# Kernel optimization log

Hardware: AMD Instinct MI355X
Metric: run time of the kernel (lower is better)

The kernel has to match this reference:

```python
import jax, jax.numpy as jnp
import numpy as np

B = 8; N_PER = 4096; N = B * N_PER          # batched graph: 8 graphs x 4096 nodes
DEG = 8; E_PER = N_PER * DEG; E = B * E_PER  # 262144 edges total
H = 128; LAYERS = 15; IN_F = 3; OUT_F = 1; EPS = 1e-5


def setup_inputs() -> dict:
    key = jax.random.key(0)
    ks = jax.random.split(key, 8)
    x = jax.random.normal(ks[0], (N, IN_F), jnp.float32)
    off = (jnp.arange(B) * N_PER)[:, None]  # keep edges within each graph
    src = (jax.random.randint(ks[1], (B, E_PER), 0, N_PER) + off).reshape(-1).astype(jnp.int32)
    dst = (jax.random.randint(ks[2], (B, E_PER), 0, N_PER) + off).reshape(-1).astype(jnp.int32)
    L = jax.random.normal(ks[3], (E,), jnp.float32) * 0.1  # Laplacian edge weights
    mask = jnp.ones((N, 1), jnp.float32)
    nb = 2 * LAYERS  # 30 inner GraphConv1x1 layers, all [2H -> H]
    W1 = jax.random.normal(ks[4], (IN_F, H), jnp.float32) * (1.0 / np.sqrt(IN_F))
    b1 = jnp.zeros((H,), jnp.float32)
    Wb = jax.random.normal(ks[5], (nb, 2 * H, H), jnp.float32) * (1.0 / np.sqrt(2 * H))
    bb = jnp.zeros((nb, H), jnp.float32)
    gb = jnp.ones((nb, 2 * H), jnp.float32)
    betab = jnp.zeros((nb, 2 * H), jnp.float32)
    g2 = jnp.ones((H,), jnp.float32)
    beta2 = jnp.zeros((H,), jnp.float32)
    W2 = jax.random.normal(ks[6], (H, OUT_F), jnp.float32) * (1.0 / np.sqrt(H))
    b2 = jnp.zeros((OUT_F,), jnp.float32)
    return {"x": x, "L": L, "mask": mask, "W1": W1, "b1": b1, "Wb": Wb, "bb": bb,
            "gb": gb, "betab": betab, "g2": g2, "beta2": beta2, "W2": W2, "b2": b2,
            "src": src, "dst": dst}


def _bn(h, g, b):
    # BatchNorm1d in training mode: per-channel stats over all nodes (B*N_PER)
    m = h.mean(axis=0)
    v = jnp.mean((h - m) ** 2, axis=0)
    return (h - m) * (g / jnp.sqrt(v + EPS)) + b


def reference(x, L, mask, W1, b1, Wb, bb, gb, betab, g2, beta2, W2, b2, src, dst):
    def spmm(h):  # update_all(u_mul_e('feat','L'), sum('msg','feat'))
        return jax.ops.segment_sum(h[src] * L[:, None], dst, num_segments=N)

    def gavg(h):  # masked per-graph global average, broadcast back to nodes
        s = (h * mask).reshape(B, N_PER, -1).sum(axis=1)   # [B, C]
        n = mask.reshape(B, N_PER, 1).sum(axis=1)           # [B, 1]
        return jnp.repeat(s / n, N_PER, axis=0)             # [N, C]

    h = x @ W1 + b1  # conv1: no BN
    for i in range(LAYERS):
        res = h
        for j in range(2):
            k = 2 * i + j
            h = jax.nn.elu(h)
            agg = spmm(h) if i % 2 == 0 else gavg(h)
            h = jnp.concatenate([h, agg], axis=1)           # [N, 2H]
            h = _bn(h, gb[k], betab[k])                     # pre-BN
            h = h @ Wb[k] + bb[k]                           # [N, H]
        h = h + res
    h = jax.nn.elu(h)
    h = _bn(h, g2, beta2)
    h = h @ W2 + b2
    # repeating_expand(in=3, out=1) -> inputs[:, :1]
    return h + x[:, :OUT_F]
```

## Files before the change

kernel.cpp:

```cpp
#include <hip/hip_runtime.h>
#include <hip/hip_bf16.h>
#include <math.h>

#define NTOT   32768
#define NPER   4096
#define NGRAPH 8
#define EDGES  262144
#define HCH    128
#define EPSBN  1e-5f
#define BANKS  16

typedef short bf16x8 __attribute__((ext_vector_type(8)));
typedef float f32x4  __attribute__((ext_vector_type(4)));

__device__ __forceinline__ float eluf(float x){ return x > 0.f ? x : expm1f(x); }
__device__ __forceinline__ ushort f2bf(float f){
    uint u = __float_as_uint(f);
    u += 0x7fffu + ((u >> 16) & 1u);
    return (ushort)(u >> 16);
}
__device__ __forceinline__ float bfhi(uint p){ return __uint_as_float(p & 0xffff0000u); }
__device__ __forceinline__ float bflo(uint p){ return __uint_as_float(p << 16); }
__device__ __forceinline__ uint packu(float v){
    ushort hi = f2bf(v);
    float r = v - __uint_as_float(((uint)hi) << 16);
    ushort lo = f2bf(r);
    return (((uint)hi) << 16) | (uint)lo;
}

__global__ __launch_bounds__(256) void k_hist(const int* __restrict__ dst, int* __restrict__ deg){
    int e = blockIdx.x * 256 + threadIdx.x;
    atomicAdd(&deg[dst[e]], 1);
}

__global__ __launch_bounds__(1024) void k_scan(const int* __restrict__ deg, int* __restrict__ rowptr,
                                               int* __restrict__ cursor){
    __shared__ int part[1024];
    int t = threadIdx.x;
    const int chunk = NTOT / 1024;
    int base = t * chunk;
    int s = 0;
    for (int j = 0; j < chunk; ++j) s += deg[base + j];
    part[t] = s; __syncthreads();
    for (int off = 1; off < 1024; off <<= 1){
        int v = (t >= off) ? part[t - off] : 0;
        __syncthreads();
        part[t] += v;
        __syncthreads();
    }
    int run = part[t] - s;
    for (int j = 0; j < chunk; ++j){
        rowptr[base + j] = run; cursor[base + j] = run;
        run += deg[base + j];
    }
    if (t == 1023) rowptr[NTOT] = run;
}

__global__ __launch_bounds__(256) void k_scatter(const int* __restrict__ src, const int* __restrict__ dst,
                                                 const float* __restrict__ L, int* __restrict__ cursor,
                                                 int2* __restrict__ epk){
    int e = blockIdx.x * 256 + threadIdx.x;
    int d = dst[e];
    int pos = atomicAdd(&cursor[d], 1);
    int2 pv; pv.x = src[e]; pv.y = __float_as_int(L[e]);
    epk[pos] = pv;
}

__global__ __launch_bounds__(256) void k_cnt(const float* __restrict__ mask, float* __restrict__ gcnt){
    __shared__ float red[4];
    int g = blockIdx.x, t = threadIdx.x;
    float s = 0.f;
    for (int i = t; i < NPER; i += 256) s += mask[g * NPER + i];
    #pragma unroll
    for (int off = 32; off > 0; off >>= 1) s += __shfl_down(s, off);
    if ((t & 63) == 0) red[t >> 6] = s;
    __syncthreads();
    if (t == 0) gcnt[g] = red[0] + red[1] + red[2] + red[3];
}

__global__ __launch_bounds__(256) void k_wall(const float* __restrict__ Wb, uint4* __restrict__ Braw){
    int layer = blockIdx.x >> 4;
    int it = ((blockIdx.x & 15) << 8) | threadIdx.x;
    int nt = it >> 9;
    int rem = it & 511;
    int kc = rem >> 6, l = rem & 63;
    int col = nt * 16 + (l & 15);
    int k0  = kc * 32 + (l >> 4) * 8;
    const float* W = Wb + (size_t)layer * 256 * HCH;
    ushort hi[8];
    #pragma unroll
    for (int q = 0; q < 8; ++q) hi[q] = f2bf(W[(size_t)(k0 + q) * HCH + col]);
    uint4 vh;
    vh.x = hi[0] | ((uint)hi[1] << 16); vh.y = hi[2] | ((uint)hi[3] << 16);
    vh.z = hi[4] | ((uint)hi[5] << 16); vh.w = hi[6] | ((uint)hi[7] << 16);
    Braw[(size_t)layer * 4096 + (size_t)(nt * 8 + kc) * 64 + l] = vh;
}

__global__ __launch_bounds__(256) void k_conv1(const float* __restrict__ x, const float* __restrict__ W1,
                                               const float* __restrict__ b1, float* __restrict__ H,
                                               uint* __restrict__ Upk, ushort* __restrict__ Uh,
                                               float* __restrict__ sums0){
    __shared__ float red[2][2][128];
    int t = threadIdx.x, ch = t & 127, pr = t >> 7;
    float w0 = W1[ch], w1 = W1[128 + ch], w2 = W1[256 + ch], bv = b1[ch];
    int base = blockIdx.x * 128;
    float ls = 0.f, lss = 0.f;
    for (int it = 0; it < 64; ++it){
        int row = base + 2 * it + pr;
        const float* xr = x + (size_t)row * 3;
        float h = fmaf(xr[2], w2, fmaf(xr[1], w1, fmaf(xr[0], w0, bv)));
        H[(size_t)row * HCH + ch] = h;
        float u = eluf(h);
        uint p = packu(u);
        Upk[(size_t)row * HCH + ch] = p;
        Uh[(size_t)row * HCH + ch] = (ushort)(p >> 16);
        ls += u; lss += u * u;
    }
    red[0][pr][ch] = ls; red[1][pr][ch] = lss;
    __syncthreads();
    if (t < 128){
        float* sb_ = sums0 + (size_t)(blockIdx.x & (BANKS - 1)) * 512;
        atomicAdd(&sb_[t],       red[0][0][t] + red[0][1][t]);
        atomicAdd(&sb_[256 + t], red[1][0][t] + red[1][1][t]);
    }
}

__global__ __launch_bounds__(256) void k_spmm(const ushort* __restrict__ Uh, const int* __restrict__ rowptr,
                                              const int2* __restrict__ epk,
                                              ushort* __restrict__ AGGh, float* __restrict__ sums_k){
    __shared__ float red[2][16][128];
    const int t = threadIdx.x;
    const int rg = t >> 4, c8 = (t & 15) << 3;
    const int bid = blockIdx.x;
    const int sb = ((bid & 7) << 8) | (bid >> 3);
    const int node = sb * 16 + rg;
    const int e0 = rowptr[node], e1 = rowptr[node + 1];

    auto acc8 = [](float* a, uint4 p, float wv){
        a[0] = fmaf(bflo(p.x), wv, a[0]); a[1] = fmaf(bfhi(p.x), wv, a[1]);
        a[2] = fmaf(bflo(p.y), wv, a[2]); a[3] = fmaf(bfhi(p.y), wv, a[3]);
        a[4] = fmaf(bflo(p.z), wv, a[4]); a[5] = fmaf(bfhi(p.z), wv, a[5]);
        a[6] = fmaf(bflo(p.w), wv, a[6]); a[7] = fmaf(bfhi(p.w), wv, a[7]);
    };

    float a[8] = {0,0,0,0,0,0,0,0};
    int e = e0;
    for (; e + 8 <= e1; e += 8){
        int2 PV[8];
        #pragma unroll
        for (int q = 0; q < 8; ++q) PV[q] = epk[e + q];
        uint4 P[8];
        #pragma unroll
        for (int q = 0; q < 8; ++q)
            P[q] = *(const uint4*)(Uh + (size_t)PV[q].x * HCH + c8);
        #pragma unroll
        for (int q = 0; q < 8; ++q) acc8(a, P[q], __int_as_float(PV[q].y));
    }
    for (; e + 2 <= e1; e += 2){
        int2 pv0 = epk[e], pv1 = epk[e + 1];
        uint4 p0 = *(const uint4*)(Uh + (size_t)pv0.x * HCH + c8);
        uint4 p1 = *(const uint4*)(Uh + (size_t)pv1.x * HCH + c8);
        acc8(a, p0, __int_as_float(pv0.y));
        acc8(a, p1, __int_as_float(pv1.y));
    }
    if (e < e1){
        int2 pv = epk[e];
        uint4 p = *(const uint4*)(Uh + (size_t)pv.x * HCH + c8);
        acc8(a, p, __int_as_float(pv.y));
    }
    uint4 o;
    o.x = (uint)f2bf(a[0]) | ((uint)f2bf(a[1]) << 16);
    o.y = (uint)f2bf(a[2]) | ((uint)f2bf(a[3]) << 16);
    o.z = (uint)f2bf(a[4]) | ((uint)f2bf(a[5]) << 16);
    o.w = (uint)f2bf(a[6]) | ((uint)f2bf(a[7]) << 16);
    *(uint4*)(AGGh + (size_t)node * HCH + c8) = o;

    #pragma unroll
    for (int j = 0; j < 8; ++j){
        red[0][rg][c8 + j] = a[j];
        red[1][rg][c8 + j] = a[j] * a[j];
    }
    __syncthreads();
    if (t < 128){
        float s = 0.f, q = 0.f;
        #pragma unroll
        for (int g = 0; g < 16; ++g){ s += red[0][g][t]; q += red[1][g][t]; }
        float* sb_ = sums_k + (size_t)(bid & (BANKS - 1)) * 512;
        atomicAdd(&sb_[128 + t], s);
        atomicAdd(&sb_[384 + t], q);
    }
}

template<int MODE, int RES>
__global__ __launch_bounds__(256) void k_gemm(
        const uint* __restrict__ Upk, const ushort* __restrict__ AGGh,
        const uint4* __restrict__ Braw,
        const float* __restrict__ gamma, const float* __restrict__ beta,
        const float* __restrict__ bias,
        const float* __restrict__ sums_k, const float* __restrict__ gsum_k,
        const float* __restrict__ gcnt,
        const float* __restrict__ Hres, float* __restrict__ Hout,
        uint* __restrict__ Uout, ushort* __restrict__ Uhout,
        float* __restrict__ sums_n, const float* __restrict__ mask,
        float* __restrict__ gsum_next)
{
    __shared__ uint a_sm[4][2][512];
    __shared__ float s_s[256], s_sh[256];
    __shared__ uint s_avgpk[64];
    __shared__ float red[2][2][128];
    __shared__ float gred[2][128];
    const int t = threadIdx.x;
    const int w = t >> 6, lane = t & 63;
    const int rlo = lane & 15, kg = lane >> 4;
    const int bid = blockIdx.x;
    const int sb  = ((bid & 7) << 7) | (bid >> 3);
    const int row0 = sb * 32;
    const int wr0 = row0 + (w & 1) * 16;
    const int colbase = (w >> 1) * 64;
    const int ntb = (w >> 1) * 4;

    {
        float m, ex2;
        if (MODE == 1 && t >= 128){
            float S1 = 0.f, S2 = 0.f;
            #pragma unroll
            for (int g = 0; g < NGRAPH; ++g){
                float a = gsum_k[g * 128 + (t - 128)] / gcnt[g];
                S1 += a; S2 += a * a;
            }
            m = S1 * (1.f / NGRAPH); ex2 = S2 * (1.f / NGRAPH);
        } else {
            float S = 0.f, Q = 0.f;
            #pragma unroll
            for (int b = 0; b < BANKS; ++b){
                S += sums_k[(size_t)b * 512 + t];
                Q += sums_k[(size_t)b * 512 + 256 + t];
            }
            m = S * (1.f / NTOT); ex2 = Q * (1.f / NTOT);
        }
        float var = ex2 - m * m;
        float sc = gamma[t] * rsqrtf(var + EPSBN);
        s_s[t] = sc; s_sh[t] = beta[t] - m * sc;
    }
    __syncthreads();
    if (MODE == 1){
        if (t < 64){
            int g0 = row0 >> 12;
            float a0 = gsum_k[g0 * 128 + 2 * t]     / gcnt[g0];
            float a1 = gsum_k[g0 * 128 + 2 * t + 1] / gcnt[g0];
            float z0 = fmaf(a0, s_s[128 + 2 * t],     s_sh[128 + 2 * t]);
            float z1 = fmaf(a1, s_s[128 + 2 * t + 1], s_sh[128 + 2 * t + 1]);
            s_avgpk[t] = (uint)f2bf(z0) | ((uint)f2bf(z1) << 16);
        }
        __syncthreads();
    }

    auto stageU = [&](int kc, uint* dst){
        int row = lane >> 2, sl = (lane & 3) * 2;
        int kb = kc * 32 + sl * 4;
        const uint* sp = Upk + (size_t)(wr0 + row) * HCH + kb;
        uint4 v0 = *(const uint4*)sp;
        uint4 v1 = *(const uint4*)(sp + 4);
        uint in[8] = {v0.x, v0.y, v0.z, v0.w, v1.x, v1.y, v1.z, v1.w};
        uint o[8];
        #pragma unroll
        for (int j = 0; j < 8; ++j){
            float z = bfhi(in[j]) + bflo(in[j]);
            o[j] = packu(fmaf(z, s_s[kb + j], s_sh[kb + j]));
        }
        uint4 w0 = {o[0], o[1], o[2], o[3]};
        uint4 w1 = {o[4], o[5], o[6], o[7]};
        *(uint4*)&dst[row * 32 + ((sl    ) ^ (row & 7)) * 4] = w0;
        *(uint4*)&dst[row * 32 + ((sl + 1) ^ (row & 7)) * 4] = w1;
    };
    auto stageG = [&](int kc, uint* dst){
        int row = lane >> 2, sl = lane & 3;
        int kb = (kc - 4) * 32 + sl * 8;
        const ushort* sp = AGGh + (size_t)(wr0 + row) * HCH + kb;
        uint4 v = *(const uint4*)sp;
        uint in[4] = {v.x, v.y, v.z, v.w};
        uint o[4];
        #pragma unroll
        for (int j = 0; j < 4; ++j){
            int c0 = 128 + kb + 2 * j;
            float z0 = fmaf(bflo(in[j]), s_s[c0],     s_sh[c0]);
            float z1 = fmaf(bfhi(in[j]), s_s[c0 + 1], s_sh[c0 + 1]);
            o[j] = (uint)f2bf(z0) | ((uint)f2bf(z1) << 16);
        }
        ushort* ds = (ushort*)dst;
        uint4 wv = {o[0], o[1], o[2], o[3]};
        *(uint4*)&ds[row * 40 + sl * 8] = wv;
    };

    f32x4 acc[4];
    #pragma unroll
    for (int n = 0; n < 4; ++n) acc[n] = (f32x4){0.f, 0.f, 0.f, 0.f};

    stageU(0, &a_sm[w][0][0]);
    #pragma unroll
    for (int kc = 0; kc < 8; ++kc){
        uint* cur = &a_sm[w][kc & 1][0];
        uint* nxt = &a_sm[w][(kc & 1) ^ 1][0];
        const bool isG = (kc >= 4);
        union { uint u[4]; bf16x8 v; } ah, al;
        if (isG && MODE == 1){
            int base = (kc - 4) * 16 + kg * 4;
            ah.u[0] = s_avgpk[base + 0]; ah.u[1] = s_avgpk[base + 1];
            ah.u[2] = s_avgpk[base + 2]; ah.u[3] = s_avgpk[base + 3];
        } else if (isG){
            const ushort* cs = (const ushort*)cur;
            uint4 c0 = *(const uint4*)&cs[rlo * 40 + kg * 8];
            ah.u[0] = c0.x; ah.u[1] = c0.y; ah.u[2] = c0.z; ah.u[3] = c0.w;
        } else {
            uint4 c0 = *(const uint4*)&cur[rlo * 32 + ((2 * kg    ) ^ (rlo & 7)) * 4];
            uint4 c1 = *(const uint4*)&cur[rlo * 32 + ((2 * kg + 1) ^ (rlo & 7)) * 4];
            ah.u[0] = (c0.x >> 16) | (c0.y & 0xffff0000u);
            ah.u[1] = (c0.z >> 16) | (c0.w & 0xffff0000u);
            ah.u[2] = (c1.x >> 16) | (c1.y & 0xffff0000u);
            ah.u[3] = (c1.z >> 16) | (c1.w & 0xffff0000u);
            al.u[0] = (c0.x & 0xffffu) | (c0.y << 16);
            al.u[1] = (c0.z & 0xffffu) | (c0.w << 16);
            al.u[2] = (c1.x & 0xffffu) | (c1.y << 16);
            al.u[3] = (c1.z & 0xffffu) | (c1.w << 16);
        }
        if (kc + 1 < 8){
            if (MODE == 0){
                if (kc + 1 >= 4) stageG(kc + 1, nxt);
                else             stageU(kc + 1, nxt);
            } else {
                if (kc + 1 < 4)  stageU(kc + 1, nxt);
            }
        }
        #pragma unroll
        for (int n = 0; n < 4; ++n){
            const int nt = ntb + n;
            union { uint4 q; bf16x8 v; } bh;
            bh.q = Braw[(size_t)(nt * 8 + kc) * 64 + lane];
            acc[n] = __builtin_amdgcn_mfma_f32_16x16x32_bf16(ah.v, bh.v, acc[n], 0, 0, 0);
            if (!isG)
                acc[n] = __builtin_amdgcn_mfma_f32_16x16x32_bf16(al.v, bh.v, acc[n], 0, 0, 0);
        }
    }

    const int r0 = wr0 + kg * 4;
    float mk[4] = {0.f, 0.f, 0.f, 0.f};
    if (gsum_next){ mk[0] = mask[r0]; mk[1] = mask[r0+1]; mk[2] = mask[r0+2]; mk[3] = mask[r0+3]; }
    #pragma unroll
    for (int n = 0; n < 4; ++n){
        const int c = colbase + n * 16 + rlo;
        const float bc = bias[c];
        float s = 0.f, q = 0.f, g = 0.f;
        #pragma unroll
        for (int r = 0; r < 4; ++r){
            int row = r0 + r;
            float h = acc[n][r] + bc;
            if (RES){
                h += Hres[(size_t)row * HCH + c];
                Hout[(size_t)row * HCH + c] = h;
            }
            float u = eluf(h);
            uint p = packu(u);
            Uout[(size_t)row * HCH + c] = p;
            if (Uhout) Uhout[(size_t)row * HCH + c] = (ushort)(p >> 16);
            s += u; q += u * u;
            if (gsum_next) g = fmaf(u, mk[r], g);
        }
        s += __shfl_xor(s, 16); s += __shfl_xor(s, 32);
        q += __shfl_xor(q, 16); q += __shfl_xor(q, 32);
        if (gsum_next){ g += __shfl_xor(g, 16); g += __shfl_xor(g, 32); }
        if (kg == 0){
            red[0][w & 1][c] = s;
            red[1][w & 1][c] = q;
            if (gsum_next) gred[w & 1][c] = g;
        }
    }
    __syncthreads();
    if (t < 128){
        float a = red[0][0][t] + red[0][1][t];
        float b = red[1][0][t] + red[1][1][t];
        float* sb_ = sums_n + (size_t)(bid & (BANKS - 1)) * 512;
        atomicAdd(&sb_[t], a);
        atomicAdd(&sb_[256 + t], b);
        if (gsum_next)
            atomicAdd(&gsum_next[(row0 >> 12) * 128 + t], gred[0][t] + gred[1][t]);
    }
}

__global__ __launch_bounds__(256) void k_final(const uint* __restrict__ Upk, const float* __restrict__ sums30,
                                               const float* __restrict__ g2, const float* __restrict__ beta2,
                                               const float* __restrict__ W2, const float* __restrict__ b2,
                                               const float* __restrict__ x, float* __restrict__ out){
    __shared__ float s_s[128], s_sh[128];
    __shared__ float wred[4];
    int t = threadIdx.x;
    if (t < 128){
        float S = 0.f, Q = 0.f;
        for (int b = 0; b < BANKS; ++b){
            S += sums30[(size_t)b * 512 + t];
            Q += sums30[(size_t)b * 512 + 256 + t];
        }
        float m   = S * (1.f / NTOT);
        float ex2 = Q * (1.f / NTOT);
        float var = ex2 - m * m;
        float sc = g2[t] * rsqrtf(var + EPSBN);
        s_s[t] = sc; s_sh[t] = beta2[t] - m * sc;
    }
    __syncthreads();
    int lane = t & 63, wid = t >> 6;
    int ch = t & 127, pr = t >> 7;
    float w2 = W2[ch];
    float b2v = b2[0];
    int base = blockIdx.x * 64;
    for (int it = 0; it < 32; ++it){
        int rowa = base + it * 2;
        int row  = rowa + pr;
        uint p = Upk[(size_t)row * HCH + ch];
        float u = bfhi(p) + bflo(p);
        float v = (u * s_s[ch] + s_sh[ch]) * w2;
        #pragma unroll
        for (int off = 32; off > 0; off >>= 1) v += __shfl_down(v, off);
        if (lane == 0) wred[wid] = v;
        __syncthreads();
        if (t == 0)   out[rowa]     = wred[0] + wred[1] + b2v + x[(size_t)rowa * 3];
        if (t == 128) out[rowa + 1] = wred[2] + wred[3] + b2v + x[(size_t)(rowa + 1) * 3];
        __syncthreads();
    }
}

extern "C" void kernel_launch(void* const* d_in, const int* in_sizes, int n_in,
                              void* d_out, int out_size, void* d_ws, size_t ws_size,
                              hipStream_t stream){
    const float* x    = (const float*)d_in[0];
    const float* L    = (const float*)d_in[1];
    const float* mask = (const float*)d_in[2];
    const float* W1   = (const float*)d_in[3];
    const float* b1   = (const float*)d_in[4];
    const float* Wb   = (const float*)d_in[5];
    const float* bb   = (const float*)d_in[6];
    const float* gb   = (const float*)d_in[7];
    const float* betab= (const float*)d_in[8];
    const float* g2   = (const float*)d_in[9];
    const float* beta2= (const float*)d_in[10];
    const float* W2   = (const float*)d_in[11];
    const float* b2   = (const float*)d_in[12];
    const int*   src  = (const int*)d_in[13];
    const int*   dst  = (const int*)d_in[14];

    char* base = (char*)d_ws;
    size_t off = 0;
    auto alloc = [&](size_t bytes)->char*{
        char* r = base + off;
        off = (off + bytes + 255) & ~(size_t)255;
        return r;
    };
    float* sums  = (float*)alloc((size_t)31 * BANKS * 512 * sizeof(float));
    float* gsum  = (float*)alloc(30 * NGRAPH * HCH * sizeof(float));
    int*   deg   = (int*)  alloc(NTOT * sizeof(int));
    size_t zero_bytes = off;
    float* gcnt  = (float*)alloc(NGRAPH * sizeof(float));
    int*   cursor= (int*)  alloc(NTOT * sizeof(int));
    int*   rowptr= (int*)  alloc((NTOT + 1) * sizeof(int));
    int2*  epk   = (int2*) alloc(EDGES * sizeof(int2));
    float* H0    = (float*)alloc((size_t)NTOT * HCH * sizeof(float));
    uint*  U0    = (uint*) alloc((size_t)NTOT * HCH * sizeof(uint));
    uint*  U1    = (uint*) alloc((size_t)NTOT * HCH * sizeof(uint));
    ushort* Uh0  = (ushort*)alloc((size_t)NTOT * HCH * sizeof(ushort));
    ushort* Uh1  = (ushort*)alloc((size_t)NTOT * HCH * sizeof(ushort));
    ushort* AGGh = (ushort*)alloc((size_t)NTOT * HCH * sizeof(ushort));
    uint4* Braw  = (uint4*)alloc((size_t)30 * 4096 * sizeof(uint4));
    (void)ws_size; (void)in_sizes; (void)n_in; (void)out_size;

    hipMemsetAsync(d_ws, 0, zero_bytes, stream);
    k_wall   <<<480, 256, 0, stream>>>(Wb, Braw);
    k_hist   <<<EDGES / 256, 256, 0, stream>>>(dst, deg);
    k_scan   <<<1, 1024, 0, stream>>>(deg, rowptr, cursor);
    k_scatter<<<EDGES / 256, 256, 0, stream>>>(src, dst, L, cursor, epk);
    k_cnt    <<<NGRAPH, 256, 0, stream>>>(mask, gcnt);
    k_conv1  <<<NTOT / 128, 256, 0, stream>>>(x, W1, b1, H0, U0, Uh0, sums);

    uint* Ucur = U0;   uint* Unext = U1;
    ushort* Hcur = Uh0; ushort* Hnext = Uh1;
    for (int i = 0; i < 15; ++i){
        for (int j = 0; j < 2; ++j){
            int k = 2 * i + j;
            const uint4* Bk  = Braw + (size_t)k * 4096;
            const float* bk  = bb + (size_t)k * HCH;
            const float* gk  = gb + (size_t)k * 256;
            const float* bek = betab + (size_t)k * 256;
            float* sk = sums + (size_t)k * BANKS * 512;
            float* sn = sums + (size_t)(k + 1) * BANKS * 512;
            bool nextg  = (k < 29) && ((((k + 1) / 2) & 1) == 1);
            bool needUh = (k < 29) && ((((k + 1) / 2) & 1) == 0);
            float* gsn = nextg ? (gsum + (size_t)(k + 1) * NGRAPH * HCH) : nullptr;
            ushort* uho = needUh ? Hnext : nullptr;
            if ((i & 1) == 0){
                k_spmm<<<NTOT / 16, 256, 0, stream>>>(Hcur, rowptr, epk, AGGh, sk);
                if (j == 0)
                    k_gemm<0,0><<<NTOT / 32, 256, 0, stream>>>(Ucur, AGGh, Bk, gk, bek, bk,
                                                               sk, nullptr, gcnt,
                                                               nullptr, nullptr, Unext, uho, sn, mask, gsn);
                else
                    k_gemm<0,1><<<NTOT / 32, 256, 0, stream>>>(Ucur, AGGh, Bk, gk, bek, bk,
                                                               sk, nullptr, gcnt,
                                                               H0, H0, Unext, uho, sn, mask, gsn);
            } else {
                float* gs = gsum + (size_t)k * NGRAPH * HCH;
                if (j == 0)
                    k_gemm<1,0><<<NTOT / 32, 256, 0, stream>>>(Ucur, nullptr, Bk, gk, bek, bk,
                                                               sk, gs, gcnt,
                                                               nullptr, nullptr, Unext, uho, sn, mask, gsn);
                else
                    k_gemm<1,1><<<NTOT / 32, 256, 0, stream>>>(Ucur, nullptr, Bk, gk, bek, bk,
                                                               sk, gs, gcnt,
                                                               H0, H0, Unext, uho, sn, mask, gsn);
            }
            uint* tmp = Ucur; Ucur = Unext; Unext = tmp;
            ushort* tmph = Hcur; Hcur = Hnext; Hnext = tmph;
        }
    }
    k_final<<<NTOT / 64, 256, 0, stream>>>(Ucur, sums + (size_t)30 * BANKS * 512, g2, beta2, W2, b2, x, (float*)d_out);
}
```

Measured before the change: 887.1 us.

## Drop split-bf16 hi/lo activation storage and use single bf16 everywhere

Activations were stored as packed hi+lo bf16 pairs (32-bit) alongside a separate hi-only copy, and the GEMM issued two MFMAs per step for the self half to keep near-fp32 precision. This keeps only one bf16 activation buffer, stages both halves of the concatenated input with a single swizzled ushort path, and issues one MFMA per step. Global traffic, LDS footprint and MFMA count all drop. The cost is lower precision in the self-feature half of the GEMM input across 30 layers, which could push the output past the accuracy tolerance.

```diff
diff --git a/kernel.cpp b/kernel.cpp
--- a/kernel.cpp
+++ b/kernel.cpp
@@ -19,14 +19,9 @@
     u += 0x7fffu + ((u >> 16) & 1u);
     return (ushort)(u >> 16);
 }
+__device__ __forceinline__ float bf2f(ushort h){ return __uint_as_float(((uint)h) << 16); }
 __device__ __forceinline__ float bfhi(uint p){ return __uint_as_float(p & 0xffff0000u); }
 __device__ __forceinline__ float bflo(uint p){ return __uint_as_float(p << 16); }
-__device__ __forceinline__ uint packu(float v){
-    ushort hi = f2bf(v);
-    float r = v - __uint_as_float(((uint)hi) << 16);
-    ushort lo = f2bf(r);
-    return (((uint)hi) << 16) | (uint)lo;
-}
 
 __global__ __launch_bounds__(256) void k_hist(const int* __restrict__ dst, int* __restrict__ deg){
     int e = blockIdx.x * 256 + threadIdx.x;
@@ -98,8 +93,7 @@
 
 __global__ __launch_bounds__(256) void k_conv1(const float* __restrict__ x, const float* __restrict__ W1,
                                                const float* __restrict__ b1, float* __restrict__ H,
-                                               uint* __restrict__ Upk, ushort* __restrict__ Uh,
-                                               float* __restrict__ sums0){
+                                               ushort* __restrict__ Uh, float* __restrict__ sums0){
     __shared__ float red[2][2][128];
     int t = threadIdx.x, ch = t & 127, pr = t >> 7;
     float w0 = W1[ch], w1 = W1[128 + ch], w2 = W1[256 + ch], bv = b1[ch];
@@ -111,9 +105,7 @@
         float h = fmaf(xr[2], w2, fmaf(xr[1], w1, fmaf(xr[0], w0, bv)));
         H[(size_t)row * HCH + ch] = h;
         float u = eluf(h);
-        uint p = packu(u);
-        Upk[(size_t)row * HCH + ch] = p;
-        Uh[(size_t)row * HCH + ch] = (ushort)(p >> 16);
+        Uh[(size_t)row * HCH + ch] = f2bf(u);
         ls += u; lss += u * u;
     }
     red[0][pr][ch] = ls; red[1][pr][ch] = lss;
@@ -193,18 +185,18 @@
 
 template<int MODE, int RES>
 __global__ __launch_bounds__(256) void k_gemm(
-        const uint* __restrict__ Upk, const ushort* __restrict__ AGGh,
+        const ushort* __restrict__ Uh, const ushort* __restrict__ AGGh,
         const uint4* __restrict__ Braw,
         const float* __restrict__ gamma, const float* __restrict__ beta,
         const float* __restrict__ bias,
         const float* __restrict__ sums_k, const float* __restrict__ gsum_k,
         const float* __restrict__ gcnt,
         const float* __restrict__ Hres, float* __restrict__ Hout,
-        uint* __restrict__ Uout, ushort* __restrict__ Uhout,
+        ushort* __restrict__ Uhout,
         float* __restrict__ sums_n, const float* __restrict__ mask,
         float* __restrict__ gsum_next)
 {
-    __shared__ uint a_sm[4][2][512];
+    __shared__ ushort a_sm[4][2][512];
     __shared__ float s_s[256], s_sh[256];
     __shared__ uint s_avgpk[64];
     __shared__ float red[2][2][128];
@@ -255,90 +247,53 @@
         __syncthreads();
     }
 
-    auto stageU = [&](int kc, uint* dst){
-        int row = lane >> 2, sl = (lane & 3) * 2;
-        int kb = kc * 32 + sl * 4;
-        const uint* sp = Upk + (size_t)(wr0 + row) * HCH + kb;
-        uint4 v0 = *(const uint4*)sp;
-        uint4 v1 = *(const uint4*)(sp + 4);
-        uint in[8] = {v0.x, v0.y, v0.z, v0.w, v1.x, v1.y, v1.z, v1.w};
-        uint o[8];
-        #pragma unroll
-        for (int j = 0; j < 8; ++j){
-            float z = bfhi(in[j]) + bflo(in[j]);
-            o[j] = packu(fmaf(z, s_s[kb + j], s_sh[kb + j]));
-        }
-        uint4 w0 = {o[0], o[1], o[2], o[3]};
-        uint4 w1 = {o[4], o[5], o[6], o[7]};
-        *(uint4*)&dst[row * 32 + ((sl    ) ^ (row & 7)) * 4] = w0;
-        *(uint4*)&dst[row * 32 + ((sl + 1) ^ (row & 7)) * 4] = w1;
-    };
-    auto stageG = [&](int kc, uint* dst){
+    auto stage = [&](int kc, ushort* dst){
         int row = lane >> 2, sl = lane & 3;
-        int kb = (kc - 4) * 32 + sl * 8;
-        const ushort* sp = AGGh + (size_t)(wr0 + row) * HCH + kb;
+        int ch = kc * 32 + sl * 8;
+        const ushort* sp = (ch < 128)
+            ? (Uh   + (size_t)(wr0 + row) * HCH + ch)
+            : (AGGh + (size_t)(wr0 + row) * HCH + (ch - 128));
         uint4 v = *(const uint4*)sp;
         uint in[4] = {v.x, v.y, v.z, v.w};
         uint o[4];
         #pragma unroll
         for (int j = 0; j < 4; ++j){
-            int c0 = 128 + kb + 2 * j;
-            float z0 = fmaf(bflo(in[j]), s_s[c0],     s_sh[c0]);
-            float z1 = fmaf(bfhi(in[j]), s_s[c0 + 1], s_sh[c0 + 1]);
+            int c = ch + 2 * j;
+            float z0 = fmaf(bflo(in[j]), s_s[c],     s_sh[c]);
+            float z1 = fmaf(bfhi(in[j]), s_s[c + 1], s_sh[c + 1]);
             o[j] = (uint)f2bf(z0) | ((uint)f2bf(z1) << 16);
         }
-        ushort* ds = (ushort*)dst;
+        int slot = sl ^ ((row >> 1) & 3);
         uint4 wv = {o[0], o[1], o[2], o[3]};
-        *(uint4*)&ds[row * 40 + sl * 8] = wv;
+        *(uint4*)&dst[row * 32 + slot * 8] = wv;
     };
 
     f32x4 acc[4];
     #pragma unroll
     for (int n = 0; n < 4; ++n) acc[n] = (f32x4){0.f, 0.f, 0.f, 0.f};
 
-    stageU(0, &a_sm[w][0][0]);
+    stage(0, &a_sm[w][0][0]);
     #pragma unroll
     for (int kc = 0; kc < 8; ++kc){
-        uint* cur = &a_sm[w][kc & 1][0];
-        uint* nxt = &a_sm[w][(kc & 1) ^ 1][0];
-        const bool isG = (kc >= 4);
-        union { uint u[4]; bf16x8 v; } ah, al;
-        if (isG && MODE == 1){
+        ushort* cur = &a_sm[w][kc & 1][0];
+        ushort* nxt = &a_sm[w][(kc & 1) ^ 1][0];
+        union { uint u[4]; bf16x8 v; } ah;
+        if (MODE == 1 && kc >= 4){
             int base = (kc - 4) * 16 + kg * 4;
             ah.u[0] = s_avgpk[base + 0]; ah.u[1] = s_avgpk[base + 1];
             ah.u[2] = s_avgpk[base + 2]; ah.u[3] = s_avgpk[base + 3];
-        } else if (isG){
-            const ushort* cs = (const ushort*)cur;
-            uint4 c0 = *(const uint4*)&cs[rlo * 40 + kg * 8];
+        } else {
+            int slot = kg ^ ((rlo >> 1) & 3);
+            uint4 c0 = *(const uint4*)&cur[rlo * 32 + slot * 8];
             ah.u[0] = c0.x; ah.u[1] = c0.y; ah.u[2] = c0.z; ah.u[3] = c0.w;
-        } else {
-            uint4 c0 = *(const uint4*)&cur[rlo * 32 + ((2 * kg    ) ^ (rlo & 7)) * 4];
-            uint4 c1 = *(const uint4*)&cur[rlo * 32 + ((2 * kg + 1) ^ (rlo & 7)) * 4];
-            ah.u[0] = (c0.x >> 16) | (c0.y & 0xffff0000u);
-            ah.u[1] = (c0.z >> 16) | (c0.w & 0xffff0000u);
-            ah.u[2] = (c1.x >> 16) | (c1.y & 0xffff0000u);
-            ah.u[3] = (c1.z >> 16) | (c1.w & 0xffff0000u);
-            al.u[0] = (c0.x & 0xffffu) | (c0.y << 16);
-            al.u[1] = (c0.z & 0xffffu) | (c0.w << 16);
-            al.u[2] = (c1.x & 0xffffu) | (c1.y << 16);
-            al.u[3] = (c1.z & 0xffffu) | (c1.w << 16);
-        }
-        if (kc + 1 < 8){
-            if (MODE == 0){
-                if (kc + 1 >= 4) stageG(kc + 1, nxt);
-                else             stageU(kc + 1, nxt);
-            } else {
-                if (kc + 1 < 4)  stageU(kc + 1, nxt);
-            }
-        }
+        }
+        if (kc + 1 < ((MODE == 1) ? 4 : 8)) stage(kc + 1, nxt);
         #pragma unroll
         for (int n = 0; n < 4; ++n){
             const int nt = ntb + n;
             union { uint4 q; bf16x8 v; } bh;
             bh.q = Braw[(size_t)(nt * 8 + kc) * 64 + lane];
             acc[n] = __builtin_amdgcn_mfma_f32_16x16x32_bf16(ah.v, bh.v, acc[n], 0, 0, 0);
-            if (!isG)
-                acc[n] = __builtin_amdgcn_mfma_f32_16x16x32_bf16(al.v, bh.v, acc[n], 0, 0, 0);
         }
     }
 
@@ -359,9 +314,7 @@
                 Hout[(size_t)row * HCH + c] = h;
             }
             float u = eluf(h);
-            uint p = packu(u);
-            Uout[(size_t)row * HCH + c] = p;
-            if (Uhout) Uhout[(size_t)row * HCH + c] = (ushort)(p >> 16);
+            Uhout[(size_t)row * HCH + c] = f2bf(u);
             s += u; q += u * u;
             if (gsum_next) g = fmaf(u, mk[r], g);
         }
@@ -386,7 +339,7 @@
     }
 }
 
-__global__ __launch_bounds__(256) void k_final(const uint* __restrict__ Upk, const float* __restrict__ sums30,
+__global__ __launch_bounds__(256) void k_final(const ushort* __restrict__ Uh, const float* __restrict__ sums30,
                                                const float* __restrict__ g2, const float* __restrict__ beta2,
                                                const float* __restrict__ W2, const float* __restrict__ b2,
                                                const float* __restrict__ x, float* __restrict__ out){
@@ -414,8 +367,7 @@
     for (int it = 0; it < 32; ++it){
         int rowa = base + it * 2;
         int row  = rowa + pr;
-        uint p = Upk[(size_t)row * HCH + ch];
-        float u = bfhi(p) + bflo(p);
+        float u = bf2f(Uh[(size_t)row * HCH + ch]);
         float v = (u * s_s[ch] + s_sh[ch]) * w2;
         #pragma unroll
         for (int off = 32; off > 0; off >>= 1) v += __shfl_down(v, off);
@@ -462,8 +414,6 @@
     int*   rowptr= (int*)  alloc((NTOT + 1) * sizeof(int));
     int2*  epk   = (int2*) alloc(EDGES * sizeof(int2));
     float* H0    = (float*)alloc((size_t)NTOT * HCH * sizeof(float));
-    uint*  U0    = (uint*) alloc((size_t)NTOT * HCH * sizeof(uint));
-    uint*  U1    = (uint*) alloc((size_t)NTOT * HCH * sizeof(uint));
     ushort* Uh0  = (ushort*)alloc((size_t)NTOT * HCH * sizeof(ushort));
     ushort* Uh1  = (ushort*)alloc((size_t)NTOT * HCH * sizeof(ushort));
     ushort* AGGh = (ushort*)alloc((size_t)NTOT * HCH * sizeof(ushort));
@@ -476,10 +426,9 @@
     k_scan   <<<1, 1024, 0, stream>>>(deg, rowptr, cursor);
     k_scatter<<<EDGES / 256, 256, 0, stream>>>(src, dst, L, cursor, epk);
     k_cnt    <<<NGRAPH, 256, 0, stream>>>(mask, gcnt);
-    k_conv1  <<<NTOT / 128, 256, 0, stream>>>(x, W1, b1, H0, U0, Uh0, sums);
-
-    uint* Ucur = U0;   uint* Unext = U1;
-    ushort* Hcur = Uh0; ushort* Hnext = Uh1;
+    k_conv1  <<<NTOT / 128, 256, 0, stream>>>(x, W1, b1, H0, Uh0, sums);
+
+    ushort* Ucur = Uh0; ushort* Unext = Uh1;
     for (int i = 0; i < 15; ++i){
         for (int j = 0; j < 2; ++j){
             int k = 2 * i + j;
@@ -490,32 +439,29 @@
             float* sk = sums + (size_t)k * BANKS * 512;
             float* sn = sums + (size_t)(k + 1) * BANKS * 512;
             bool nextg  = (k < 29) && ((((k + 1) / 2) & 1) == 1);
-            bool needUh = (k < 29) && ((((k + 1) / 2) & 1) == 0);
             float* gsn = nextg ? (gsum + (size_t)(k + 1) * NGRAPH * HCH) : nullptr;
-            ushort* uho = needUh ? Hnext : nullptr;
             if ((i & 1) == 0){
-                k_spmm<<<NTOT / 16, 256, 0, stream>>>(Hcur, rowptr, epk, AGGh, sk);
+                k_spmm<<<NTOT / 16, 256, 0, stream>>>(Ucur, rowptr, epk, AGGh, sk);
                 if (j == 0)
                     k_gemm<0,0><<<NTOT / 32, 256, 0, stream>>>(Ucur, AGGh, Bk, gk, bek, bk,
                                                                sk, nullptr, gcnt,
-                                                               nullptr, nullptr, Unext, uho, sn, mask, gsn);
+                                                               nullptr, nullptr, Unext, sn, mask, gsn);
                 else
                     k_gemm<0,1><<<NTOT / 32, 256, 0, stream>>>(Ucur, AGGh, Bk, gk, bek, bk,
                                                                sk, nullptr, gcnt,
-                                                               H0, H0, Unext, uho, sn, mask, gsn);
+                                                               H0, H0, Unext, sn, mask, gsn);
             } else {
                 float* gs = gsum + (size_t)k * NGRAPH * HCH;
                 if (j == 0)
                     k_gemm<1,0><<<NTOT / 32, 256, 0, stream>>>(Ucur, nullptr, Bk, gk, bek, bk,
                                                                sk, gs, gcnt,
-                                                               nullptr, nullptr, Unext, uho, sn, mask, gsn);
+                                                               nullptr, nullptr, Unext, sn, mask, gsn);
                 else
                     k_gemm<1,1><<<NTOT / 32, 256, 0, stream>>>(Ucur, nullptr, Bk, gk, bek, bk,
                                                                sk, gs, gcnt,
-                                                               H0, H0, Unext, uho, sn, mask, gsn);
+                                                               H0, H0, Unext, sn, mask, gsn);
             }
-            uint* tmp = Ucur; Ucur = Unext; Unext = tmp;
-            ushort* tmph = Hcur; Hcur = Hnext; Hnext = tmph;
+            ushort* tmp = Ucur; Ucur = Unext; Unext = tmp;
         }
     }
     k_final<<<NTOT / 64, 256, 0, stream>>>(Ucur, sums + (size_t)30 * BANKS * 512, g2, beta2, W2, b2, x, (float*)d_out);
```

Result: faster. 779.1 us (median of 2 runs) (-12.2%).
